# Kernel tuning notes

Hardware: AMD Instinct MI355X
Metric: run time of the kernel (lower is better)

The kernel has to match this reference:

```python
import jax, jax.numpy as jnp
import numpy as np


def _sage_layer(h_src, src, dst, n_dst, Wself, Wneigh, b):
    # DGL SAGEConv('mean'): out = fc_self(h_dst) + fc_neigh(mean_{u->v} h_src[u]) + bias
    msg = jax.ops.segment_sum(h_src[src], dst, num_segments=n_dst)          # [n_dst, d]
    deg = jax.ops.segment_sum(jnp.ones(src.shape, h_src.dtype), dst, num_segments=n_dst)
    mean = msg / jnp.maximum(deg, 1.0)[:, None]
    h_dst = h_src[:n_dst]  # DGL block convention: dst nodes are first n_dst src nodes
    return h_dst @ Wself.T + mean @ Wneigh.T + b


def setup_inputs() -> dict:
    key = jax.random.key(0)
    ks = jax.random.split(key, 12)
    d_in, d_h, d_out = 128, 128, 64
    N0, N1, N2, N3 = 500000, 100000, 20000, 5000
    E0, E1, E2 = 2000000, 400000, 100000
    s = 0.05
    return {
        "input_feats": jax.random.normal(ks[0], (N0, d_in), jnp.float32),
        "src0": jax.random.randint(ks[1], (E0,), 0, N0),
        "dst0": jax.random.randint(ks[2], (E0,), 0, N1),
        "src1": jax.random.randint(ks[3], (E1,), 0, N1),
        "dst1": jax.random.randint(ks[4], (E1,), 0, N2),
        "src2": jax.random.randint(ks[5], (E2,), 0, N2),
        "dst2": jax.random.randint(ks[6], (E2,), 0, N3),
        "n_dst0": N1, "n_dst1": N2, "n_dst2": N3,
        "Wself0": jax.random.normal(ks[7], (d_h, d_in), jnp.float32) * s,
        "Wneigh0": jax.random.normal(ks[8], (d_h, d_in), jnp.float32) * s,
        "b0": jnp.zeros((d_h,), jnp.float32),
        "Wself1": jax.random.normal(ks[9], (d_h, d_h), jnp.float32) * s,
        "Wneigh1": jax.random.normal(ks[10], (d_h, d_h), jnp.float32) * s,
        "b1": jnp.zeros((d_h,), jnp.float32),
        "Wself2": jax.random.normal(ks[11], (d_out, d_h), jnp.float32) * s,
        "Wneigh2": jax.random.normal(jax.random.fold_in(key, 99), (d_out, d_h), jnp.float32) * s,
        "b2": jnp.zeros((d_out,), jnp.float32),
    }


def reference(input_feats, src0, dst0, src1, dst1, src2, dst2,
              n_dst0, n_dst1, n_dst2,
              Wself0, Wneigh0, b0, Wself1, Wneigh1, b1, Wself2, Wneigh2, b2):
    # Layer 0 (+ FeatureShuffle == identity on a single device) + relu (dropout=0)
    h = _sage_layer(input_feats, src0, dst0, n_dst0, Wself0, Wneigh0, b0)
    h = jax.nn.relu(h)
    # Layer 1 + relu
    h = _sage_layer(h, src1, dst1, n_dst1, Wself1, Wneigh1, b1)
    h = jax.nn.relu(h)
    # Layer 2 (output, no activation)
    h = _sage_layer(h, src2, dst2, n_dst2, Wself2, Wneigh2, b2)
    return h
```

## Files before the change

kernel.cpp:

```cpp
#include <hip/hip_runtime.h>

#define K_DIM 128
#define NTOT   125000
#define RPB    512
#define NB     245
#define SRC_BITS 19
#define SRC_MASK 0x7FFFF

typedef __attribute__((ext_vector_type(8))) short bf16x8;
typedef __attribute__((ext_vector_type(8))) unsigned short u16x8;
typedef __attribute__((ext_vector_type(4))) float f32x4;

static __device__ __forceinline__ unsigned short f2bf(float f) {
    union { float f; unsigned u; } v; v.f = f;
    unsigned r = v.u + 0x7FFF + ((v.u >> 16) & 1);
    return (unsigned short)(r >> 16);
}
static __device__ __forceinline__ float bf2f(unsigned short b) {
    union { unsigned u; float f; } v; v.u = ((unsigned)b) << 16;
    return v.f;
}

static __device__ __forceinline__ void conv_feat_part(
    const float* __restrict__ feats, unsigned short* __restrict__ feats_bf,
    int c0, int c1, int b0, int ncb, int b, int t)
{
    int stride = ncb * 256;
    for (long i = c0 + (long)(b - b0) * 256 + t; i < c1; i += stride) {
        float4 a = reinterpret_cast<const float4*>(feats)[2 * i];
        float4 c = reinterpret_cast<const float4*>(feats)[2 * i + 1];
        uint4 o;
        o.x = (unsigned)f2bf(a.x) | ((unsigned)f2bf(a.y) << 16);
        o.y = (unsigned)f2bf(a.z) | ((unsigned)f2bf(a.w) << 16);
        o.z = (unsigned)f2bf(c.x) | ((unsigned)f2bf(c.y) << 16);
        o.w = (unsigned)f2bf(c.z) | ((unsigned)f2bf(c.w) << 16);
        reinterpret_cast<uint4*>(feats_bf)[i] = o;
    }
}

__global__ __launch_bounds__(256)
void prep1_kernel(const int* __restrict__ d0, const int* __restrict__ d1,
                  const int* __restrict__ d2, int E0, int E1, int Etot,
                  int* __restrict__ bucket_cnt,
                  const float* __restrict__ w0s, const float* __restrict__ w0n,
                  const float* __restrict__ w1s, const float* __restrict__ w1n,
                  const float* __restrict__ w2s, const float* __restrict__ w2n,
                  unsigned short* __restrict__ wbf)
{
    __shared__ int hist[256];
    int b = blockIdx.x;
    int t = threadIdx.x;

    if (b < 512) {
        hist[t] = 0;
        __syncthreads();
        int stride = 512 * 256;
        for (int e = b * 256 + t; e < Etot; e += stride) {
            int row;
            if (e < E0)           row = d0[e];
            else if (e < E0 + E1) row = 100000 + d1[e - E0];
            else                  row = 120000 + d2[e - E0 - E1];
            atomicAdd(&hist[row >> 9], 1);
        }
        __syncthreads();
        if (t < NB && hist[t]) atomicAdd(&bucket_cnt[t], hist[t]);
    } else {
        int idx = (b - 512) * 256 + t;
        if (idx >= 81920) return;
        if (idx < 16384) {
            wbf[idx] = f2bf(w0s[idx]);
        } else if (idx < 32768) {
            int i = idx - 16384; float v = w0n[i];
            unsigned short hi = f2bf(v);
            wbf[16384 + i] = hi;
            wbf[32768 + i] = f2bf(v - bf2f(hi));
        } else if (idx < 49152) {
            int i = idx - 32768;
            wbf[49152 + i] = f2bf(w1s[i]);
        } else if (idx < 65536) {
            int i = idx - 49152; float v = w1n[i];
            unsigned short hi = f2bf(v);
            wbf[65536 + i] = hi;
            wbf[81920 + i] = f2bf(v - bf2f(hi));
        } else if (idx < 73728) {
            int i = idx - 65536;
            wbf[98304 + i] = f2bf(w2s[i]);
        } else {
            int i = idx - 73728; float v = w2n[i];
            unsigned short hi = f2bf(v);
            wbf[106496 + i] = hi;
            wbf[114688 + i] = f2bf(v - bf2f(hi));
        }
    }
}

__global__ __launch_bounds__(256)
void bucket_scan_kernel(const int* __restrict__ bucket_cnt,
                        int* __restrict__ bucket_base,
                        int* __restrict__ bucket_cursor, int Etot)
{
    __shared__ int sm[256];
    int t = threadIdx.x;
    int v = (t < NB) ? bucket_cnt[t] : 0;
    sm[t] = v;
    __syncthreads();
    for (int s = 1; s < 256; s <<= 1) {
        int a = (t >= s) ? sm[t - s] : 0;
        __syncthreads();
        sm[t] += a;
        __syncthreads();
    }
    int excl = sm[t] - v;
    if (t < NB) { bucket_base[t] = excl; bucket_cursor[t] = excl; }
    if (t == 0) bucket_base[NB] = Etot;
}

#define CHUNK 4096
__global__ __launch_bounds__(256)
void scatter_conv_kernel(const int* __restrict__ s0, const int* __restrict__ d0,
                         const int* __restrict__ s1, const int* __restrict__ d1,
                         const int* __restrict__ s2, const int* __restrict__ d2,
                         int E0, int E1, int Etot,
                         int* __restrict__ bucket_cursor,
                         int* __restrict__ ebuf,
                         const float* __restrict__ feats,
                         unsigned short* __restrict__ feats_bf,
                         int cmid, int SCB, int ncb)
{
    __shared__ int hist[256];
    __shared__ int start[256];
    int t = threadIdx.x;
    int b = blockIdx.x;

    if (b >= SCB) {
        conv_feat_part(feats, feats_bf, 0, cmid, SCB, ncb, b, t);
        return;
    }

    int base = b * CHUNK;
    hist[t] = 0;
    __syncthreads();

    #pragma unroll
    for (int i = 0; i < CHUNK / 256; ++i) {
        int e = base + i * 256 + t;
        if (e < Etot) {
            int row;
            if (e < E0)           row = d0[e];
            else if (e < E0 + E1) row = 100000 + d1[e - E0];
            else                  row = 120000 + d2[e - E0 - E1];
            atomicAdd(&hist[row >> 9], 1);
        }
    }
    __syncthreads();
    if (t < NB) {
        int c = hist[t];
        start[t] = c ? atomicAdd(&bucket_cursor[t], c) : 0;
    }
    __syncthreads();
    hist[t] = 0;
    __syncthreads();

    #pragma unroll
    for (int i = 0; i < CHUNK / 256; ++i) {
        int e = base + i * 256 + t;
        if (e < Etot) {
            int row, src;
            if (e < E0)           { row = d0[e];                    src = s0[e]; }
            else if (e < E0 + E1) { row = 100000 + d1[e - E0];      src = s1[e - E0]; }
            else                  { row = 120000 + d2[e - E0 - E1]; src = s2[e - E0 - E1]; }
            int bb = row >> 9;
            int pos = start[bb] + atomicAdd(&hist[bb], 1);
            ebuf[pos] = ((row & (RPB - 1)) << SRC_BITS) | src;
        }
    }
}

__global__ __launch_bounds__(256)
void fill_conv_kernel(const int* __restrict__ ebuf,
                      const int* __restrict__ bucket_base,
                      int* __restrict__ rowstart,
                      int* __restrict__ csr, int Etot,
                      const float* __restrict__ feats,
                      unsigned short* __restrict__ feats_bf,
                      int cmid, int ctot, int ncb)
{
    __shared__ int hist[RPB];
    __shared__ int ps[256];
    __shared__ int rst[RPB];

    int t = threadIdx.x;
    int b = blockIdx.x;

    if (b >= NB) {
        conv_feat_part(feats, feats_bf, cmid, ctot, NB, ncb, b, t);
        return;
    }

    int e0 = bucket_base[b], e1 = bucket_base[b + 1];
    int row0 = b << 9;
    int nrows = min(RPB, NTOT - row0);

    hist[t] = 0; hist[t + 256] = 0;
    __syncthreads();
    for (int e = e0 + t; e < e1; e += 256)
        atomicAdd(&hist[(unsigned)ebuf[e] >> SRC_BITS], 1);
    __syncthreads();

    int a0 = hist[2 * t], a1 = hist[2 * t + 1];
    int pv = a0 + a1;
    ps[t] = pv;
    __syncthreads();
    for (int s = 1; s < 256; s <<= 1) {
        int a = (t >= s) ? ps[t - s] : 0;
        __syncthreads();
        ps[t] += a;
        __syncthreads();
    }
    int pe = ps[t] - pv;
    rst[2 * t] = pe;
    rst[2 * t + 1] = pe + a0;
    __syncthreads();

    if (2 * t < nrows)     rowstart[row0 + 2 * t]     = e0 + rst[2 * t];
    if (2 * t + 1 < nrows) rowstart[row0 + 2 * t + 1] = e0 + rst[2 * t + 1];
    if (b == NB - 1 && t == 0) rowstart[NTOT] = Etot;
    hist[2 * t] = rst[2 * t];
    hist[2 * t + 1] = rst[2 * t + 1];
    __syncthreads();

    for (int e = e0 + t; e < e1; e += 256) {
        unsigned p = (unsigned)ebuf[e];
        int off = atomicAdd(&hist[p >> SRC_BITS], 1);
        csr[e0 + off] = p & SRC_MASK;
    }
}

__global__ __launch_bounds__(256)
void gather_mean_f32_kernel(const float* __restrict__ h,
                            const int* __restrict__ csr,
                            const int* __restrict__ rs,
                            unsigned short* __restrict__ msgb, int n)
{
    long gid = (long)blockIdx.x * 256 + threadIdx.x;
    int g = (int)(gid >> 5);
    int lane = (int)(gid & 31);
    if (g >= n) return;

    int s0 = rs[g], s1 = rs[g + 1];
    float4 acc = make_float4(0.f, 0.f, 0.f, 0.f);
    int e = s0;
    for (; e + 4 <= s1; e += 4) {
        int i0 = csr[e], i1 = csr[e + 1], i2 = csr[e + 2], i3 = csr[e + 3];
        float4 v0 = reinterpret_cast<const float4*>(h + (long)i0 * K_DIM)[lane];
        float4 v1 = reinterpret_cast<const float4*>(h + (long)i1 * K_DIM)[lane];
        float4 v2 = reinterpret_cast<const float4*>(h + (long)i2 * K_DIM)[lane];
        float4 v3 = reinterpret_cast<const float4*>(h + (long)i3 * K_DIM)[lane];
        acc.x += (v0.x + v1.x) + (v2.x + v3.x);
        acc.y += (v0.y + v1.y) + (v2.y + v3.y);
        acc.z += (v0.z + v1.z) + (v2.z + v3.z);
        acc.w += (v0.w + v1.w) + (v2.w + v3.w);
    }
    for (; e < s1; ++e) {
        int i0 = csr[e];
        float4 v0 = reinterpret_cast<const float4*>(h + (long)i0 * K_DIM)[lane];
        acc.x += v0.x; acc.y += v0.y; acc.z += v0.z; acc.w += v0.w;
    }
    float rd = 1.0f / fmaxf((float)(s1 - s0), 1.0f);
    ushort4 o;
    o.x = f2bf(acc.x * rd); o.y = f2bf(acc.y * rd);
    o.z = f2bf(acc.z * rd); o.w = f2bf(acc.w * rd);
    reinterpret_cast<ushort4*>(msgb + (long)g * K_DIM)[lane] = o;
}

__global__ __launch_bounds__(256)
void gather_mean_bf_kernel(const unsigned short* __restrict__ hb,
                           const int* __restrict__ csr,
                           const int* __restrict__ rs,
                           unsigned short* __restrict__ msgb, int n)
{
    long gid = (long)blockIdx.x * 256 + threadIdx.x;
    int g = (int)(gid >> 4);
    int lane = (int)(gid & 15);
    if (g >= n) return;

    int s0 = rs[g], s1 = rs[g + 1];
    float a[8] = {0.f, 0.f, 0.f, 0.f, 0.f, 0.f, 0.f, 0.f};
    const unsigned short* hb_l = hb + lane * 8;

    int e = s0;
    for (; e + 8 <= s1; e += 8) {
        int idx[8];
        #pragma unroll
        for (int i = 0; i < 8; ++i) idx[i] = csr[e + i];
        #pragma unroll
        for (int i = 0; i < 8; ++i) {
            u16x8 v = *reinterpret_cast<const u16x8*>(hb_l + (long)idx[i] * K_DIM);
            #pragma unroll
            for (int j = 0; j < 8; ++j) a[j] += bf2f(v[j]);
        }
    }
    for (; e < s1; ++e) {
        u16x8 v = *reinterpret_cast<const u16x8*>(hb_l + (long)csr[e] * K_DIM);
        #pragma unroll
        for (int j = 0; j < 8; ++j) a[j] += bf2f(v[j]);
    }
    float rd = 1.0f / fmaxf((float)(s1 - s0), 1.0f);
    u16x8 o;
    #pragma unroll
    for (int j = 0; j < 8; ++j) o[j] = f2bf(a[j] * rd);
    *reinterpret_cast<u16x8*>(msgb + (long)g * K_DIM + lane * 8) = o;
}

template<int NCOL, bool RELU, bool WRITE_BF>
__global__ __launch_bounds__(256, 3)
void sage_gemm_mfma(const float* __restrict__ h,
                    const unsigned short* __restrict__ msgb,
                    const unsigned short* __restrict__ wsb,
                    const unsigned short* __restrict__ wnh,
                    const unsigned short* __restrict__ wnl,
                    const float* __restrict__ bias,
                    float* __restrict__ out,
                    unsigned short* __restrict__ outb,
                    int n, int nf32)
{
    constexpr int NCB = NCOL / 16;
    __shared__ bf16x8 Ah[8][64];
    __shared__ bf16x8 Al[8][64];
    __shared__ bf16x8 Ms[8][64];
    __shared__ bf16x8 Bs[NCB][64];
    __shared__ bf16x8 Bh[NCB][64];
    __shared__ bf16x8 Bl[NCB][64];

    const int t    = threadIdx.x;
    const int lane = t & 63;
    const int w    = t >> 6;
    const int row0 = blockIdx.x * 128;

    f32x4 acc[2][NCB];
    #pragma unroll
    for (int rf = 0; rf < 2; ++rf)
        #pragma unroll
        for (int cb = 0; cb < NCB; ++cb)
            acc[rf][cb] = (f32x4){0.f, 0.f, 0.f, 0.f};

    const int arow   = t & 127;
    const int ah2    = t >> 7;
    const int grow_a = min(row0 + arow, n - 1);
    const int arb    = arow >> 4;

    for (int kc = 0; kc < 128; kc += 32) {
        __syncthreads();
        #pragma unroll
        for (int i = 0; i < 2; ++i) {
            int hh = ah2 * 2 + i;
            const float* src = h + (long)grow_a * 128 + kc + hh * 8;
            float4 x = *reinterpret_cast<const float4*>(src);
            float4 y = *reinterpret_cast<const float4*>(src + 4);
            float xs[8] = {x.x, x.y, x.z, x.w, y.x, y.y, y.z, y.w};
            bf16x8 hi8, lo8;
            #pragma unroll
            for (int j = 0; j < 8; ++j) {
                unsigned short hu = f2bf(xs[j]);
                hi8[j] = (short)hu;
                lo8[j] = (short)f2bf(xs[j] - bf2f(hu));
            }
            int li = hh * 16 + (arow & 15);
            Ah[arb][li] = hi8;
            Al[arb][li] = lo8;
            Ms[arb][li] = *reinterpret_cast<const bf16x8*>(
                              msgb + (long)grow_a * 128 + kc + hh * 8);
        }
        if (NCOL == 128) {
            int col = t & 127, h2 = t >> 7;
            #pragma unroll
            for (int i = 0; i < 2; ++i) {
                int hh = h2 * 2 + i;
                int li = hh * 16 + (col & 15);
                int cb = col >> 4;
                long o = (long)col * 128 + kc + hh * 8;
                Bs[cb][li] = *reinterpret_cast<const bf16x8*>(wsb + o);
                Bh[cb][li] = *reinterpret_cast<const bf16x8*>(wnh + o);
                Bl[cb][li] = *reinterpret_cast<const bf16x8*>(wnl + o);
            }
        } else {
            int col = t & 63, hh = t >> 6;
            int li = hh * 16 + (col & 15);
            int cb = col >> 4;
            long o = (long)col * 128 + kc + hh * 8;
            Bs[cb][li] = *reinterpret_cast<const bf16x8*>(wsb + o);
            Bh[cb][li] = *reinterpret_cast<const bf16x8*>(wnh + o);
            Bl[cb][li] = *reinterpret_cast<const bf16x8*>(wnl + o);
        }
        __syncthreads();

        bf16x8 a0h = Ah[2 * w][lane],     a0l = Al[2 * w][lane],     m0 = Ms[2 * w][lane];
        bf16x8 a1h = Ah[2 * w + 1][lane], a1l = Al[2 * w + 1][lane], m1 = Ms[2 * w + 1][lane];
        #pragma unroll
        for (int cb = 0; cb < NCB; ++cb) {
            bf16x8 bs = Bs[cb][lane];
            bf16x8 bh = Bh[cb][lane];
            bf16x8 bl = Bl[cb][lane];
            acc[0][cb] = __builtin_amdgcn_mfma_f32_16x16x32_bf16(a0h, bs, acc[0][cb], 0, 0, 0);
            acc[0][cb] = __builtin_amdgcn_mfma_f32_16x16x32_bf16(a0l, bs, acc[0][cb], 0, 0, 0);
            acc[0][cb] = __builtin_amdgcn_mfma_f32_16x16x32_bf16(m0,  bh, acc[0][cb], 0, 0, 0);
            acc[0][cb] = __builtin_amdgcn_mfma_f32_16x16x32_bf16(m0,  bl, acc[0][cb], 0, 0, 0);
            acc[1][cb] = __builtin_amdgcn_mfma_f32_16x16x32_bf16(a1h, bs, acc[1][cb], 0, 0, 0);
            acc[1][cb] = __builtin_amdgcn_mfma_f32_16x16x32_bf16(a1l, bs, acc[1][cb], 0, 0, 0);
            acc[1][cb] = __builtin_amdgcn_mfma_f32_16x16x32_bf16(m1,  bh, acc[1][cb], 0, 0, 0);
            acc[1][cb] = __builtin_amdgcn_mfma_f32_16x16x32_bf16(m1,  bl, acc[1][cb], 0, 0, 0);
        }
    }

    #pragma unroll
    for (int rf = 0; rf < 2; ++rf) {
        #pragma unroll
        for (int cb = 0; cb < NCB; ++cb) {
            int col = cb * 16 + (lane & 15);
            float bv = bias[col];
            #pragma unroll
            for (int r = 0; r < 4; ++r) {
                int grow = row0 + w * 32 + rf * 16 + (lane >> 4) * 4 + r;
                if (grow < n) {
                    float v = acc[rf][cb][r] + bv;
                    if (RELU) v = fmaxf(v, 0.f);
                    if (grow < nf32) out[(long)grow * NCOL + col] = v;
                    if (WRITE_BF) outb[(long)grow * NCOL + col] = f2bf(v);
                }
            }
        }
    }
}

extern "C" void kernel_launch(void* const* d_in, const int* in_sizes, int n_in,
                              void* d_out, int out_size, void* d_ws, size_t ws_size,
                              hipStream_t stream)
{
    const float* feats   = (const float*)d_in[0];
    const int*   src0    = (const int*)d_in[1];
    const int*   dst0    = (const int*)d_in[2];
    const int*   src1    = (const int*)d_in[3];
    const int*   dst1    = (const int*)d_in[4];
    const int*   src2    = (const int*)d_in[5];
    const int*   dst2    = (const int*)d_in[6];
    const float* Wself0  = (const float*)d_in[10];
    const float* Wneigh0 = (const float*)d_in[11];
    const float* b0      = (const float*)d_in[12];
    const float* Wself1  = (const float*)d_in[13];
    const float* Wneigh1 = (const float*)d_in[14];
    const float* b1      = (const float*)d_in[15];
    const float* Wself2  = (const float*)d_in[16];
    const float* Wneigh2 = (const float*)d_in[17];
    const float* b2      = (const float*)d_in[18];

    const int E0 = in_sizes[1];
    const int E1 = in_sizes[3];
    const int E2 = in_sizes[5];
    const int Etot = E0 + E1 + E2;
    const int N1 = 100000, N2 = 20000, N3 = 5000;

    char* base = (char*)d_ws;
    const bool bfp = ws_size >= 164500000ull;

    unsigned short* feats_bf; float* h1; unsigned short* h1b;
    float* h2; unsigned short* h2b;
    unsigned short* msgb; int* ebuf; int* csr; int* rowstart;
    int* bcnt; int* bbase; int* bcur; unsigned short* wbf;

    if (bfp) {
        feats_bf = (unsigned short*)base;
        h1   = (float*)base;
        h1b  = (unsigned short*)(base + 51200000);
        h2   = (float*)(base + 76800000);
        h2b  = (unsigned short*)(base + 87040000);
        msgb = (unsigned short*)(base + 128000000);
        csr      = (int*)(base + 153600000);
        rowstart = (int*)(base + 163600000);
        bcnt     = (int*)(base + 164100224);
        bbase    = bcnt + 256;
        bcur     = bbase + 256;
        wbf      = (unsigned short*)(base + 164103296);
    } else {
        feats_bf = nullptr;
        h1   = (float*)base;
        h1b  = nullptr;
        h2   = (float*)(base + 51200000);
        h2b  = nullptr;
        msgb = (unsigned short*)(base + 61440000);
        csr      = (int*)(base + 87040000);
        rowstart = (int*)(base + 97040000);
        bcnt     = (int*)(base + 97540224);
        bbase    = bcnt + 256;
        bcur     = bbase + 256;
        wbf      = (unsigned short*)(base + 97543296);
    }
    ebuf = (int*)msgb;

    const int SCB  = (Etot + CHUNK - 1) / CHUNK;
    const int NCV  = bfp ? 1024 : 0;
    const int CTOT = bfp ? 8000000 : 0;
    const int CMID = CTOT / 2;

    hipMemsetAsync(bcnt, 0, 1024, stream);
    prep1_kernel<<<832, 256, 0, stream>>>(
        dst0, dst1, dst2, E0, E1, Etot, bcnt,
        Wself0, Wneigh0, Wself1, Wneigh1, Wself2, Wneigh2, wbf);
    bucket_scan_kernel<<<1, 256, 0, stream>>>(bcnt, bbase, bcur, Etot);
    scatter_conv_kernel<<<SCB + NCV, 256, 0, stream>>>(
        src0, dst0, src1, dst1, src2, dst2, E0, E1, Etot, bcur, ebuf,
        feats, feats_bf, CMID, SCB, NCV);
    fill_conv_kernel<<<NB + NCV, 256, 0, stream>>>(
        ebuf, bbase, rowstart, csr, Etot, feats, feats_bf, CMID, CTOT, NCV);

    if (bfp) {
        gather_mean_bf_kernel<<<(N1 * 16 + 255) / 256, 256, 0, stream>>>(
            feats_bf, csr, rowstart, msgb, N1);
        sage_gemm_mfma<128, true, true><<<(N1 + 127) / 128, 256, 0, stream>>>(
            feats, msgb, wbf, wbf + 16384, wbf + 32768, b0, h1, h1b, N1, N2);
        gather_mean_bf_kernel<<<(N2 * 16 + 255) / 256, 256, 0, stream>>>(
            h1b, csr, rowstart + 100000, msgb, N2);
        sage_gemm_mfma<128, true, true><<<(N2 + 127) / 128, 256, 0, stream>>>(
            h1, msgb, wbf + 49152, wbf + 65536, wbf + 81920, b1, h2, h2b, N2, N3);
        gather_mean_bf_kernel<<<(N3 * 16 + 255) / 256, 256, 0, stream>>>(
            h2b, csr, rowstart + 120000, msgb, N3);
        sage_gemm_mfma<64, false, false><<<(N3 + 127) / 128, 256, 0, stream>>>(
            h2, msgb, wbf + 98304, wbf + 106496, wbf + 114688, b2,
            (float*)d_out, nullptr, N3, N3);
    } else {
        gather_mean_f32_kernel<<<(N1 * 32 + 255) / 256, 256, 0, stream>>>(
            feats, csr, rowstart, msgb, N1);
        sage_gemm_mfma<128, true, false><<<(N1 + 127) / 128, 256, 0, stream>>>(
            feats, msgb, wbf, wbf + 16384, wbf + 32768, b0, h1, nullptr, N1, N1);
        gather_mean_f32_kernel<<<(N2 * 32 + 255) / 256, 256, 0, stream>>>(
            h1, csr, rowstart + 100000, msgb, N2);
        sage_gemm_mfma<128, true, false><<<(N2 + 127) / 128, 256, 0, stream>>>(
            h1, msgb, wbf + 49152, wbf + 65536, wbf + 81920, b1, h2, nullptr, N2, N2);
        gather_mean_f32_kernel<<<(N3 * 32 + 255) / 256, 256, 0, stream>>>(
            h2, csr, rowstart + 120000, msgb, N3);
        sage_gemm_mfma<64, false, false><<<(N3 + 127) / 128, 256, 0, stream>>>(
            h2, msgb, wbf + 98304, wbf + 106496, wbf + 114688, b2,
            (float*)d_out, nullptr, N3, N3);
    }
}
```

Before: 342.7 us.

## Fuse graph-build kernels into one cooperative kernel with work-stealing feature conversion

Replaces the memset, histogram, scan, scatter and CSR-fill launches with a single cooperative kernel that separates the phases with grid-wide syncs. The fp32-to-bf16 feature conversion is split across the three phases and handed out in grains through atomic cursors, so idle blocks in each phase pick it up. The aim is to remove launch gaps and even out load between the index-building work and the conversion. In exchange it adds grid.sync costs, and it requires all 1024 blocks to be co-resident.

```diff
diff --git a/kernel.cpp b/kernel.cpp
--- a/kernel.cpp
+++ b/kernel.cpp
@@ -1,4 +1,7 @@
 #include <hip/hip_runtime.h>
+#include <hip/hip_cooperative_groups.h>
+
+namespace cg = cooperative_groups;
 
 #define K_DIM 128
 #define NTOT   125000
@@ -6,6 +9,9 @@
 #define NB     245
 #define SRC_BITS 19
 #define SRC_MASK 0x7FFFF
+#define CHUNK 4096
+#define NBLK_BUILD 1024
+#define GRAIN 8192
 
 typedef __attribute__((ext_vector_type(8))) short bf16x8;
 typedef __attribute__((ext_vector_type(8))) unsigned short u16x8;
@@ -21,218 +27,215 @@
     return v.f;
 }
 
-static __device__ __forceinline__ void conv_feat_part(
-    const float* __restrict__ feats, unsigned short* __restrict__ feats_bf,
-    int c0, int c1, int b0, int ncb, int b, int t)
-{
-    int stride = ncb * 256;
-    for (long i = c0 + (long)(b - b0) * 256 + t; i < c1; i += stride) {
-        float4 a = reinterpret_cast<const float4*>(feats)[2 * i];
-        float4 c = reinterpret_cast<const float4*>(feats)[2 * i + 1];
-        uint4 o;
-        o.x = (unsigned)f2bf(a.x) | ((unsigned)f2bf(a.y) << 16);
-        o.y = (unsigned)f2bf(a.z) | ((unsigned)f2bf(a.w) << 16);
-        o.z = (unsigned)f2bf(c.x) | ((unsigned)f2bf(c.y) << 16);
-        o.w = (unsigned)f2bf(c.z) | ((unsigned)f2bf(c.w) << 16);
-        reinterpret_cast<uint4*>(feats_bf)[i] = o;
-    }
-}
+static __device__ __forceinline__ void conv_one(
+    const float* __restrict__ feats, unsigned short* __restrict__ fbf, long i)
+{
+    float4 x = reinterpret_cast<const float4*>(feats)[2 * i];
+    float4 y = reinterpret_cast<const float4*>(feats)[2 * i + 1];
+    uint4 o;
+    o.x = (unsigned)f2bf(x.x) | ((unsigned)f2bf(x.y) << 16);
+    o.y = (unsigned)f2bf(x.z) | ((unsigned)f2bf(x.w) << 16);
+    o.z = (unsigned)f2bf(y.x) | ((unsigned)f2bf(y.y) << 16);
+    o.w = (unsigned)f2bf(y.z) | ((unsigned)f2bf(y.w) << 16);
+    reinterpret_cast<uint4*>(fbf)[i] = o;
+}
+
+static __device__ void conv_pull(const float* __restrict__ feats,
+                                 unsigned short* __restrict__ fbf,
+                                 int lo, int hi, int* __restrict__ cursor,
+                                 int* convbase_s, int t)
+{
+    if (hi <= lo) return;
+    while (true) {
+        if (t == 0) *convbase_s = atomicAdd(cursor, GRAIN);
+        __syncthreads();
+        int base = *convbase_s;
+        __syncthreads();
+        if (lo + base >= hi) break;
+        int end = (lo + base + GRAIN < hi) ? (lo + base + GRAIN) : hi;
+        for (int i = lo + base + t; i < end; i += 256)
+            conv_one(feats, fbf, i);
+    }
+}
+
+static __device__ __forceinline__ void conv_w_item(
+    int idx,
+    const float* __restrict__ w0s, const float* __restrict__ w0n,
+    const float* __restrict__ w1s, const float* __restrict__ w1n,
+    const float* __restrict__ w2s, const float* __restrict__ w2n,
+    unsigned short* __restrict__ wbf)
+{
+    if (idx >= 81920) return;
+    if (idx < 16384) {
+        wbf[idx] = f2bf(w0s[idx]);
+    } else if (idx < 32768) {
+        int i = idx - 16384; float v = w0n[i];
+        unsigned short hi = f2bf(v);
+        wbf[16384 + i] = hi;
+        wbf[32768 + i] = f2bf(v - bf2f(hi));
+    } else if (idx < 49152) {
+        int i = idx - 32768;
+        wbf[49152 + i] = f2bf(w1s[i]);
+    } else if (idx < 65536) {
+        int i = idx - 49152; float v = w1n[i];
+        unsigned short hi = f2bf(v);
+        wbf[65536 + i] = hi;
+        wbf[81920 + i] = f2bf(v - bf2f(hi));
+    } else if (idx < 73728) {
+        int i = idx - 65536;
+        wbf[98304 + i] = f2bf(w2s[i]);
+    } else {
+        int i = idx - 73728; float v = w2n[i];
+        unsigned short hi = f2bf(v);
+        wbf[106496 + i] = hi;
+        wbf[114688 + i] = f2bf(v - bf2f(hi));
+    }
+}
+
+struct BuildArgs {
+    const int *s0, *d0, *s1, *d1, *s2, *d2;
+    int E0, E1, Etot;
+    int *bcnt, *bbase, *bcur, *ebuf, *rowstart, *csr;
+    const float *w0s, *w0n, *w1s, *w1n, *w2s, *w2n;
+    unsigned short *wbf;
+    const float *feats;
+    unsigned short *feats_bf;
+    int C1, C2, CTOT;
+};
 
 __global__ __launch_bounds__(256)
-void prep1_kernel(const int* __restrict__ d0, const int* __restrict__ d1,
-                  const int* __restrict__ d2, int E0, int E1, int Etot,
-                  int* __restrict__ bucket_cnt,
-                  const float* __restrict__ w0s, const float* __restrict__ w0n,
-                  const float* __restrict__ w1s, const float* __restrict__ w1n,
-                  const float* __restrict__ w2s, const float* __restrict__ w2n,
-                  unsigned short* __restrict__ wbf)
-{
-    __shared__ int hist[256];
-    int b = blockIdx.x;
-    int t = threadIdx.x;
-
-    if (b < 512) {
-        hist[t] = 0;
+void build_coop_kernel(BuildArgs a)
+{
+    cg::grid_group grid = cg::this_grid();
+    __shared__ int shA[RPB];
+    __shared__ int shB[256];
+    __shared__ int shC[RPB];
+    __shared__ int convbase;
+
+    const int t = threadIdx.x;
+    const int b = blockIdx.x;
+
+    if (b == 0) a.bcnt[t] = 0;
+    grid.sync();
+
+    shA[t] = 0;
+    __syncthreads();
+    for (int e = b * 256 + t; e < a.Etot; e += NBLK_BUILD * 256) {
+        int row;
+        if (e < a.E0)           row = a.d0[e];
+        else if (e < a.E0 + a.E1) row = 100000 + a.d1[e - a.E0];
+        else                    row = 120000 + a.d2[e - a.E0 - a.E1];
+        atomicAdd(&shA[row >> 9], 1);
+    }
+    __syncthreads();
+    if (t < NB && shA[t]) atomicAdd(&a.bcnt[t], shA[t]);
+    if (b >= 1 && b < 321)
+        conv_w_item((b - 1) * 256 + t, a.w0s, a.w0n, a.w1s, a.w1n, a.w2s, a.w2n, a.wbf);
+    conv_pull(a.feats, a.feats_bf, 0, a.C1, &a.bcnt[250], &convbase, t);
+    grid.sync();
+
+    if (b == 0) {
+        int v = (t < NB) ? a.bcnt[t] : 0;
+        shB[t] = v;
         __syncthreads();
-        int stride = 512 * 256;
-        for (int e = b * 256 + t; e < Etot; e += stride) {
-            int row;
-            if (e < E0)           row = d0[e];
-            else if (e < E0 + E1) row = 100000 + d1[e - E0];
-            else                  row = 120000 + d2[e - E0 - E1];
-            atomicAdd(&hist[row >> 9], 1);
-        }
-        __syncthreads();
-        if (t < NB && hist[t]) atomicAdd(&bucket_cnt[t], hist[t]);
-    } else {
-        int idx = (b - 512) * 256 + t;
-        if (idx >= 81920) return;
-        if (idx < 16384) {
-            wbf[idx] = f2bf(w0s[idx]);
-        } else if (idx < 32768) {
-            int i = idx - 16384; float v = w0n[i];
-            unsigned short hi = f2bf(v);
-            wbf[16384 + i] = hi;
-            wbf[32768 + i] = f2bf(v - bf2f(hi));
-        } else if (idx < 49152) {
-            int i = idx - 32768;
-            wbf[49152 + i] = f2bf(w1s[i]);
-        } else if (idx < 65536) {
-            int i = idx - 49152; float v = w1n[i];
-            unsigned short hi = f2bf(v);
-            wbf[65536 + i] = hi;
-            wbf[81920 + i] = f2bf(v - bf2f(hi));
-        } else if (idx < 73728) {
-            int i = idx - 65536;
-            wbf[98304 + i] = f2bf(w2s[i]);
-        } else {
-            int i = idx - 73728; float v = w2n[i];
-            unsigned short hi = f2bf(v);
-            wbf[106496 + i] = hi;
-            wbf[114688 + i] = f2bf(v - bf2f(hi));
-        }
-    }
-}
-
-__global__ __launch_bounds__(256)
-void bucket_scan_kernel(const int* __restrict__ bucket_cnt,
-                        int* __restrict__ bucket_base,
-                        int* __restrict__ bucket_cursor, int Etot)
-{
-    __shared__ int sm[256];
-    int t = threadIdx.x;
-    int v = (t < NB) ? bucket_cnt[t] : 0;
-    sm[t] = v;
-    __syncthreads();
-    for (int s = 1; s < 256; s <<= 1) {
-        int a = (t >= s) ? sm[t - s] : 0;
-        __syncthreads();
-        sm[t] += a;
-        __syncthreads();
-    }
-    int excl = sm[t] - v;
-    if (t < NB) { bucket_base[t] = excl; bucket_cursor[t] = excl; }
-    if (t == 0) bucket_base[NB] = Etot;
-}
-
-#define CHUNK 4096
-__global__ __launch_bounds__(256)
-void scatter_conv_kernel(const int* __restrict__ s0, const int* __restrict__ d0,
-                         const int* __restrict__ s1, const int* __restrict__ d1,
-                         const int* __restrict__ s2, const int* __restrict__ d2,
-                         int E0, int E1, int Etot,
-                         int* __restrict__ bucket_cursor,
-                         int* __restrict__ ebuf,
-                         const float* __restrict__ feats,
-                         unsigned short* __restrict__ feats_bf,
-                         int cmid, int SCB, int ncb)
-{
-    __shared__ int hist[256];
-    __shared__ int start[256];
-    int t = threadIdx.x;
-    int b = blockIdx.x;
-
-    if (b >= SCB) {
-        conv_feat_part(feats, feats_bf, 0, cmid, SCB, ncb, b, t);
-        return;
-    }
-
-    int base = b * CHUNK;
-    hist[t] = 0;
-    __syncthreads();
-
-    #pragma unroll
-    for (int i = 0; i < CHUNK / 256; ++i) {
-        int e = base + i * 256 + t;
-        if (e < Etot) {
-            int row;
-            if (e < E0)           row = d0[e];
-            else if (e < E0 + E1) row = 100000 + d1[e - E0];
-            else                  row = 120000 + d2[e - E0 - E1];
-            atomicAdd(&hist[row >> 9], 1);
-        }
-    }
-    __syncthreads();
-    if (t < NB) {
-        int c = hist[t];
-        start[t] = c ? atomicAdd(&bucket_cursor[t], c) : 0;
-    }
-    __syncthreads();
-    hist[t] = 0;
-    __syncthreads();
-
-    #pragma unroll
-    for (int i = 0; i < CHUNK / 256; ++i) {
-        int e = base + i * 256 + t;
-        if (e < Etot) {
-            int row, src;
-            if (e < E0)           { row = d0[e];                    src = s0[e]; }
-            else if (e < E0 + E1) { row = 100000 + d1[e - E0];      src = s1[e - E0]; }
-            else                  { row = 120000 + d2[e - E0 - E1]; src = s2[e - E0 - E1]; }
-            int bb = row >> 9;
-            int pos = start[bb] + atomicAdd(&hist[bb], 1);
-            ebuf[pos] = ((row & (RPB - 1)) << SRC_BITS) | src;
-        }
-    }
-}
-
-__global__ __launch_bounds__(256)
-void fill_conv_kernel(const int* __restrict__ ebuf,
-                      const int* __restrict__ bucket_base,
-                      int* __restrict__ rowstart,
-                      int* __restrict__ csr, int Etot,
-                      const float* __restrict__ feats,
-                      unsigned short* __restrict__ feats_bf,
-                      int cmid, int ctot, int ncb)
-{
-    __shared__ int hist[RPB];
-    __shared__ int ps[256];
-    __shared__ int rst[RPB];
-
-    int t = threadIdx.x;
-    int b = blockIdx.x;
-
-    if (b >= NB) {
-        conv_feat_part(feats, feats_bf, cmid, ctot, NB, ncb, b, t);
-        return;
-    }
-
-    int e0 = bucket_base[b], e1 = bucket_base[b + 1];
-    int row0 = b << 9;
-    int nrows = min(RPB, NTOT - row0);
-
-    hist[t] = 0; hist[t + 256] = 0;
-    __syncthreads();
-    for (int e = e0 + t; e < e1; e += 256)
-        atomicAdd(&hist[(unsigned)ebuf[e] >> SRC_BITS], 1);
-    __syncthreads();
-
-    int a0 = hist[2 * t], a1 = hist[2 * t + 1];
-    int pv = a0 + a1;
-    ps[t] = pv;
-    __syncthreads();
-    for (int s = 1; s < 256; s <<= 1) {
-        int a = (t >= s) ? ps[t - s] : 0;
-        __syncthreads();
-        ps[t] += a;
-        __syncthreads();
-    }
-    int pe = ps[t] - pv;
-    rst[2 * t] = pe;
-    rst[2 * t + 1] = pe + a0;
-    __syncthreads();
-
-    if (2 * t < nrows)     rowstart[row0 + 2 * t]     = e0 + rst[2 * t];
-    if (2 * t + 1 < nrows) rowstart[row0 + 2 * t + 1] = e0 + rst[2 * t + 1];
-    if (b == NB - 1 && t == 0) rowstart[NTOT] = Etot;
-    hist[2 * t] = rst[2 * t];
-    hist[2 * t + 1] = rst[2 * t + 1];
-    __syncthreads();
-
-    for (int e = e0 + t; e < e1; e += 256) {
-        unsigned p = (unsigned)ebuf[e];
-        int off = atomicAdd(&hist[p >> SRC_BITS], 1);
-        csr[e0 + off] = p & SRC_MASK;
+        for (int s = 1; s < 256; s <<= 1) {
+            int x = (t >= s) ? shB[t - s] : 0;
+            __syncthreads();
+            shB[t] += x;
+            __syncthreads();
+        }
+        int excl = shB[t] - v;
+        if (t < NB) { a.bbase[t] = excl; a.bcur[t] = excl; }
+        if (t == 0) a.bbase[NB] = a.Etot;
+    }
+    grid.sync();
+
+    {
+        int nchunk = (a.Etot + CHUNK - 1) / CHUNK;
+        for (int ch = b; ch < nchunk; ch += NBLK_BUILD) {
+            int basee = ch * CHUNK;
+            shA[t] = 0;
+            __syncthreads();
+            #pragma unroll
+            for (int i = 0; i < CHUNK / 256; ++i) {
+                int e = basee + i * 256 + t;
+                if (e < a.Etot) {
+                    int row;
+                    if (e < a.E0)             row = a.d0[e];
+                    else if (e < a.E0 + a.E1) row = 100000 + a.d1[e - a.E0];
+                    else                      row = 120000 + a.d2[e - a.E0 - a.E1];
+                    atomicAdd(&shA[row >> 9], 1);
+                }
+            }
+            __syncthreads();
+            if (t < NB) {
+                int c = shA[t];
+                shB[t] = c ? atomicAdd(&a.bcur[t], c) : 0;
+            }
+            __syncthreads();
+            shA[t] = 0;
+            __syncthreads();
+            #pragma unroll
+            for (int i = 0; i < CHUNK / 256; ++i) {
+                int e = basee + i * 256 + t;
+                if (e < a.Etot) {
+                    int row, src;
+                    if (e < a.E0)             { row = a.d0[e];                        src = a.s0[e]; }
+                    else if (e < a.E0 + a.E1) { row = 100000 + a.d1[e - a.E0];        src = a.s1[e - a.E0]; }
+                    else                      { row = 120000 + a.d2[e - a.E0 - a.E1]; src = a.s2[e - a.E0 - a.E1]; }
+                    int bb = row >> 9;
+                    int pos = shB[bb] + atomicAdd(&shA[bb], 1);
+                    a.ebuf[pos] = ((row & (RPB - 1)) << SRC_BITS) | src;
+                }
+            }
+            __syncthreads();
+        }
+        conv_pull(a.feats, a.feats_bf, a.C1, a.C2, &a.bcnt[251], &convbase, t);
+    }
+    grid.sync();
+
+    {
+        for (int bk = b; bk < NB; bk += NBLK_BUILD) {
+            int e0 = a.bbase[bk], e1 = a.bbase[bk + 1];
+            int row0 = bk << 9;
+            int nrows = (RPB < NTOT - row0) ? RPB : (NTOT - row0);
+
+            shA[t] = 0; shA[t + 256] = 0;
+            __syncthreads();
+            for (int e = e0 + t; e < e1; e += 256)
+                atomicAdd(&shA[(unsigned)a.ebuf[e] >> SRC_BITS], 1);
+            __syncthreads();
+
+            int a0 = shA[2 * t], a1 = shA[2 * t + 1];
+            int pv = a0 + a1;
+            shB[t] = pv;
+            __syncthreads();
+            for (int s = 1; s < 256; s <<= 1) {
+                int x = (t >= s) ? shB[t - s] : 0;
+                __syncthreads();
+                shB[t] += x;
+                __syncthreads();
+            }
+            int pe = shB[t] - pv;
+            shC[2 * t] = pe;
+            shC[2 * t + 1] = pe + a0;
+            __syncthreads();
+
+            if (2 * t < nrows)     a.rowstart[row0 + 2 * t]     = e0 + shC[2 * t];
+            if (2 * t + 1 < nrows) a.rowstart[row0 + 2 * t + 1] = e0 + shC[2 * t + 1];
+            if (bk == NB - 1 && t == 0) a.rowstart[NTOT] = a.Etot;
+            shA[2 * t] = shC[2 * t];
+            shA[2 * t + 1] = shC[2 * t + 1];
+            __syncthreads();
+
+            for (int e = e0 + t; e < e1; e += 256) {
+                unsigned p = (unsigned)a.ebuf[e];
+                int off = atomicAdd(&shA[p >> SRC_BITS], 1);
+                a.csr[e0 + off] = p & SRC_MASK;
+            }
+            __syncthreads();
+        }
+        conv_pull(a.feats, a.feats_bf, a.C2, a.CTOT, &a.bcnt[252], &convbase, t);
     }
 }
 
@@ -496,21 +499,20 @@
     }
     ebuf = (int*)msgb;
 
-    const int SCB  = (Etot + CHUNK - 1) / CHUNK;
-    const int NCV  = bfp ? 1024 : 0;
-    const int CTOT = bfp ? 8000000 : 0;
-    const int CMID = CTOT / 2;
-
-    hipMemsetAsync(bcnt, 0, 1024, stream);
-    prep1_kernel<<<832, 256, 0, stream>>>(
-        dst0, dst1, dst2, E0, E1, Etot, bcnt,
-        Wself0, Wneigh0, Wself1, Wneigh1, Wself2, Wneigh2, wbf);
-    bucket_scan_kernel<<<1, 256, 0, stream>>>(bcnt, bbase, bcur, Etot);
-    scatter_conv_kernel<<<SCB + NCV, 256, 0, stream>>>(
-        src0, dst0, src1, dst1, src2, dst2, E0, E1, Etot, bcur, ebuf,
-        feats, feats_bf, CMID, SCB, NCV);
-    fill_conv_kernel<<<NB + NCV, 256, 0, stream>>>(
-        ebuf, bbase, rowstart, csr, Etot, feats, feats_bf, CMID, CTOT, NCV);
+    BuildArgs ba;
+    ba.s0 = src0; ba.d0 = dst0; ba.s1 = src1; ba.d1 = dst1; ba.s2 = src2; ba.d2 = dst2;
+    ba.E0 = E0; ba.E1 = E1; ba.Etot = Etot;
+    ba.bcnt = bcnt; ba.bbase = bbase; ba.bcur = bcur;
+    ba.ebuf = ebuf; ba.rowstart = rowstart; ba.csr = csr;
+    ba.w0s = Wself0; ba.w0n = Wneigh0; ba.w1s = Wself1; ba.w1n = Wneigh1;
+    ba.w2s = Wself2; ba.w2n = Wneigh2; ba.wbf = wbf;
+    ba.feats = feats; ba.feats_bf = feats_bf;
+    if (bfp) { ba.C1 = 2500000; ba.C2 = 5500000; ba.CTOT = 8000000; }
+    else     { ba.C1 = 0;       ba.C2 = 0;       ba.CTOT = 0; }
+
+    void* params[1] = { &ba };
+    hipLaunchCooperativeKernel((void*)build_coop_kernel,
+                               dim3(NBLK_BUILD), dim3(256), params, 0, stream);
 
     if (bfp) {
         gather_mean_bf_kernel<<<(N1 * 16 + 255) / 256, 256, 0, stream>>>(
```

After: 845.2 us. +146.6%, slower.
